# Optimization experiments

Measured on AMD Instinct MI355X. Metric: run time of the kernel, lower is better.

Reference implementation:

```python
import jax, jax.numpy as jnp
import numpy as np

N = 100000
E = 1600000
IN_DIM, H1, H2 = 64, 128, 64


def gcn_conv(x, edge_index, W, b, n_nodes):
    """PyG-style GCNConv: add self-loops, symmetric normalization, x@W, scatter-add, +bias."""
    src, dst = edge_index[0], edge_index[1]
    loop = jnp.arange(n_nodes)
    src = jnp.concatenate([src, loop])
    dst = jnp.concatenate([dst, loop])
    deg = jax.ops.segment_sum(jnp.ones_like(src, dtype=x.dtype), dst, num_segments=n_nodes)
    dinv = jax.lax.rsqrt(deg)  # deg >= 1 due to self loops
    norm = dinv[src] * dinv[dst]  # [E+N]
    xw = x @ W  # [N, out] - transform before gather (out <= in keeps traffic low)
    msg = xw[src] * norm[:, None]  # [E+N, out]
    out = jax.ops.segment_sum(msg, dst, num_segments=n_nodes)
    return out + b


def setup_inputs() -> dict:
    key = jax.random.key(0)
    ks = jax.random.split(key, 8)
    x = jax.random.normal(ks[0], (N, IN_DIM), dtype=jnp.float32)
    edge_index = jax.random.randint(ks[1], (2, E), 0, N, dtype=jnp.int64)
    W1 = jax.random.normal(ks[2], (IN_DIM, H1), dtype=jnp.float32) / np.sqrt(IN_DIM)
    b1 = jnp.zeros((H1,), dtype=jnp.float32)
    W2 = jax.random.normal(ks[3], (H1, H2), dtype=jnp.float32) / np.sqrt(H1)
    b2 = jnp.zeros((H2,), dtype=jnp.float32)
    Wfc = jax.random.normal(ks[4], (H2, 1), dtype=jnp.float32) / np.sqrt(H2)
    bfc = jnp.zeros((1,), dtype=jnp.float32)
    return {"x": x, "edge_index": edge_index, "W1": W1, "b1": b1,
            "W2": W2, "b2": b2, "Wfc": Wfc, "bfc": bfc}


def reference(x, edge_index, W1, b1, W2, b2, Wfc, bfc):
    h = jax.nn.relu(gcn_conv(x, edge_index, W1, b1, N))
    h = jax.nn.relu(gcn_conv(h, edge_index, W2, b2, N))
    return (h @ Wfc + bfc).reshape(-1)  # [N]
```

## Files before the change

kernel.cpp:

```cpp
#include <hip/hip_runtime.h>


constexpr int NN = 100000;
constexpr int NE = 1600000;
constexpr int D0 = 64;
constexpr int D1 = 128;
constexpr int D2 = 64;
constexpr int NB = (NN + 255) / 256;
constexpr int TILE = 8192;
constexpr int H1STRIDE = 132;

typedef unsigned short u16;
typedef unsigned int u32;
typedef __attribute__((ext_vector_type(8))) short short8;
typedef __attribute__((ext_vector_type(4))) float f32x4;
typedef _Float16 h4 __attribute__((ext_vector_type(4)));


__global__ __launch_bounds__(256) void k_zero_b(int* __restrict__ g) {
    int i = blockIdx.x * 256 + threadIdx.x;
    if (i < 512) g[i] = 0;
}

__global__ __launch_bounds__(256) void k_bcount(const int* __restrict__ dst,
                                                int* __restrict__ gbcnt) {
    __shared__ int cnt_s[NB];
    int tid = threadIdx.x;
    int e0 = blockIdx.x * TILE;
    int ecnt = NE - e0 < TILE ? NE - e0 : TILE;
    for (int i = tid; i < NB; i += 256) cnt_s[i] = 0;
    __syncthreads();
    for (int i = tid; i < ecnt; i += 256)
        atomicAdd(&cnt_s[dst[e0 + i] >> 8], 1);
    __syncthreads();
    for (int i = tid; i < NB; i += 256) {
        int c = cnt_s[i];
        if (c) atomicAdd(&gbcnt[i], c);
    }
}

__global__ __launch_bounds__(512) void k_scan_bsum(const int* __restrict__ gbcnt,
                                                   int* __restrict__ bsum,
                                                   int* __restrict__ gcur) {
    __shared__ int s[512];
    int tid = threadIdx.x;
    int v = (tid < NB) ? gbcnt[tid] : 0;
    s[tid] = v;
    __syncthreads();
#pragma unroll
    for (int off = 1; off < 512; off <<= 1) {
        int t = (tid >= off) ? s[tid - off] : 0;
        __syncthreads();
        s[tid] += t;
        __syncthreads();
    }
    int ex = s[tid] - v;
    if (tid <= NB) bsum[tid] = ex;
    if (tid < NB) gcur[tid] = ex;
}

__global__ __launch_bounds__(256) void k_part(const int* __restrict__ src,
                                              const int* __restrict__ dst,
                                              int* __restrict__ gcur,
                                              unsigned* __restrict__ packed) {
    __shared__ int cnt_s[NB];
    __shared__ int gbase_s[NB];
    __shared__ int cur_s[NB];
    int tid = threadIdx.x;
    int e0 = blockIdx.x * TILE;
    int ecnt = NE - e0 < TILE ? NE - e0 : TILE;
    for (int i = tid; i < NB; i += 256) cnt_s[i] = 0;
    __syncthreads();
    for (int i = tid; i < ecnt; i += 256)
        atomicAdd(&cnt_s[dst[e0 + i] >> 8], 1);
    __syncthreads();
    for (int i = tid; i < NB; i += 256) {
        int c = cnt_s[i];
        gbase_s[i] = c ? atomicAdd(&gcur[i], c) : 0;
        cur_s[i] = 0;
    }
    __syncthreads();
    for (int i = tid; i < ecnt; i += 256) {
        int d = dst[e0 + i];
        int s = src[e0 + i];
        int b = d >> 8;
        int slot = atomicAdd(&cur_s[b], 1);
        packed[gbase_s[b] + slot] = ((unsigned)(d & 255) << 24) | (unsigned)s;
    }
}

__global__ __launch_bounds__(256) void k_bucket(const int* __restrict__ bsum,
                                                const unsigned* __restrict__ packed,
                                                int* __restrict__ rowptr,
                                                float* __restrict__ dinv,
                                                int* __restrict__ col) {
    __shared__ int hist[256];
    __shared__ int s[256];
    __shared__ int cur[256];
    int b = blockIdx.x;
    int tid = threadIdx.x;
    int e0 = bsum[b], e1 = bsum[b + 1];
    hist[tid] = 0;
    __syncthreads();
    for (int e = e0 + tid; e < e1; e += 256)
        atomicAdd(&hist[packed[e] >> 24], 1);
    __syncthreads();
    int v = hist[tid];
    int n = (b << 8) + tid;
    if (n < NN) dinv[n] = rsqrtf((float)(v + 1));
    s[tid] = v;
    __syncthreads();
#pragma unroll
    for (int off = 1; off < 256; off <<= 1) {
        int t = (tid >= off) ? s[tid - off] : 0;
        __syncthreads();
        s[tid] += t;
        __syncthreads();
    }
    int base = e0 + s[tid] - v;
    if (n <= NN) rowptr[n] = base;
    cur[tid] = base;
    __syncthreads();
    for (int e = e0 + tid; e < e1; e += 256) {
        unsigned p = packed[e];
        int pos = atomicAdd(&cur[p >> 24], 1);
        col[pos] = (int)((p & 0xFFFFFFu) << 7);
    }
}


__device__ __forceinline__ float4 scale4(const float4& a, float s) {
    return float4{a.x * s, a.y * s, a.z * s, a.w * s};
}

__device__ __forceinline__ void addh8(float4& a, float4& b, uint4 u) {
    h4 h0 = *(h4*)&u.x;
    h4 h1 = *(h4*)&u.z;
    a.x += (float)h0[0]; a.y += (float)h0[1]; a.z += (float)h0[2]; a.w += (float)h0[3];
    b.x += (float)h1[0]; b.y += (float)h1[1]; b.z += (float)h1[2]; b.w += (float)h1[3];
}

__device__ __forceinline__ uint2 packh4(const float4& v) {
    h4 h;
    h[0] = (_Float16)v.x; h[1] = (_Float16)v.y;
    h[2] = (_Float16)v.z; h[3] = (_Float16)v.w;
    return *(uint2*)&h;
}

__device__ __forceinline__ void xor_reduce8(float4& a, float4& b, int mask) {
    a.x += __shfl_xor(a.x, mask, 64);
    a.y += __shfl_xor(a.y, mask, 64);
    a.z += __shfl_xor(a.z, mask, 64);
    a.w += __shfl_xor(a.w, mask, 64);
    b.x += __shfl_xor(b.x, mask, 64);
    b.y += __shfl_xor(b.y, mask, 64);
    b.z += __shfl_xor(b.z, mask, 64);
    b.w += __shfl_xor(b.w, mask, 64);
}

__device__ __forceinline__ u16 f2bf(float f) {
    u32 u = __float_as_uint(f);
    return (u16)((u + 0x7fffu + ((u >> 16) & 1u)) >> 16);
}
__device__ __forceinline__ float bf2f(u16 h) {
    return __uint_as_float(((u32)h) << 16);
}

__global__ __launch_bounds__(256) void k_prescale(const float* __restrict__ x,
                                                  const float* __restrict__ dinv,
                                                  u16* __restrict__ xs) {
    int i = blockIdx.x * 256 + threadIdx.x;
    if (i >= NN * 16) return;
    float di = dinv[i >> 4];
    ((uint2*)xs)[i] = packh4(scale4(((const float4*)x)[i], di));
}

__global__ __launch_bounds__(256) void k_gather1x(const int* __restrict__ rowptr,
                                                  const int* __restrict__ colb,
                                                  const u16* __restrict__ xs,
                                                  const float* __restrict__ dinv,
                                                  float* __restrict__ agg) {
    int wave = (blockIdx.x * 256 + threadIdx.x) >> 6;
    int lane = threadIdx.x & 63;
    if (wave >= NN) return;
    int f8 = lane & 7;
    int es = lane >> 3;
    int r0 = rowptr[wave], r1 = rowptr[wave + 1];
    const char* xsb = (const char*)xs + f8 * 16;
    float4 accA{0, 0, 0, 0}, accB{0, 0, 0, 0};
    if (es == 0) addh8(accA, accB, *(const uint4*)(xsb + (size_t)wave * 128));
    int e = r0 + es;
    for (; e + 8 < r1; e += 16) {
        int c0 = colb[e];
        int c1 = colb[e + 8];
        uint4 v0 = *(const uint4*)(xsb + c0);
        uint4 v1 = *(const uint4*)(xsb + c1);
        addh8(accA, accB, v0);
        addh8(accA, accB, v1);
    }
    for (; e < r1; e += 8)
        addh8(accA, accB, *(const uint4*)(xsb + colb[e]));
    xor_reduce8(accA, accB, 8);
    xor_reduce8(accA, accB, 16);
    xor_reduce8(accA, accB, 32);
    if (es == 0) {
        float di = dinv[wave];
        float4* ag = (float4*)agg + (size_t)wave * 16 + f8 * 2;
        ag[0] = scale4(accA, di);
        ag[1] = scale4(accB, di);
    }
}

__global__ __launch_bounds__(256) void k_splitW(const float* __restrict__ W1,
                                                const float* __restrict__ W2,
                                                u16* __restrict__ W1h, u16* __restrict__ W1l,
                                                u16* __restrict__ W2h, u16* __restrict__ W2l) {
    int i = blockIdx.x * 256 + threadIdx.x;
    if (i >= 8192) return;
    int j = i & 7;
    int l = (i >> 3) & 63;
    int ts = i >> 9;
    int kf = ((l >> 4) << 3) + j;
    int cl = l & 15;
    {
        int s = ts >> 3, t = ts & 7;
        float w = W1[(s * 32 + kf) * D1 + t * 16 + cl];
        u16 h = f2bf(w);
        W1h[i] = h;
        W1l[i] = f2bf(w - bf2f(h));
    }
    {
        int s = ts >> 2, t = ts & 3;
        float w = W2[(s * 32 + kf) * D2 + t * 16 + cl];
        u16 h = f2bf(w);
        W2h[i] = h;
        W2l[i] = f2bf(w - bf2f(h));
    }
}

__global__ __launch_bounds__(256) void k_gemm12(const float* __restrict__ agg,
                                                const u16* __restrict__ W1h,
                                                const u16* __restrict__ W1l,
                                                const float* __restrict__ b1,
                                                const u16* __restrict__ W2h,
                                                const u16* __restrict__ W2l,
                                                const float* __restrict__ dinv,
                                                u16* __restrict__ y2) {
    __shared__ u32 h1s[64 * H1STRIDE];
    int tid = threadIdx.x;
    int l = tid & 63;
    int wv = tid >> 6;
    int n_base = blockIdx.x * 64;
    int row_a = l & 15;
    int kg = (l >> 4) << 3;
    int crow = (l >> 4) * 4;

    short8 Ah[2], Al[2];
#pragma unroll
    for (int s = 0; s < 2; ++s) {
        int an = n_base + wv * 16 + row_a;
        if (an >= NN) an = NN - 1;
        const float* ap = agg + (size_t)an * D0 + s * 32 + kg;
        f32x4 v0 = *(const f32x4*)ap;
        f32x4 v1 = *(const f32x4*)(ap + 4);
#pragma unroll
        for (int j = 0; j < 4; ++j) {
            u16 h0 = f2bf(v0[j]);
            Ah[s][j] = (short)h0;
            Al[s][j] = (short)f2bf(v0[j] - bf2f(h0));
            u16 h1b = f2bf(v1[j]);
            Ah[s][j + 4] = (short)h1b;
            Al[s][j + 4] = (short)f2bf(v1[j] - bf2f(h1b));
        }
    }
#pragma unroll
    for (int t = 0; t < 8; ++t) {
        f32x4 acc = {0.f, 0.f, 0.f, 0.f};
#pragma unroll
        for (int s = 0; s < 2; ++s) {
            short8 Bh = *(const short8*)(W1h + ((size_t)(s * 8 + t) * 64 + l) * 8);
            short8 Bl = *(const short8*)(W1l + ((size_t)(s * 8 + t) * 64 + l) * 8);
            acc = __builtin_amdgcn_mfma_f32_16x16x32_bf16(Ah[s], Bh, acc, 0, 0, 0);
            acc = __builtin_amdgcn_mfma_f32_16x16x32_bf16(Ah[s], Bl, acc, 0, 0, 0);
            acc = __builtin_amdgcn_mfma_f32_16x16x32_bf16(Al[s], Bh, acc, 0, 0, 0);
        }
        float bb = b1[t * 16 + (l & 15)];
        int kcol = t * 16 + (l & 15);
#pragma unroll
        for (int r = 0; r < 4; ++r) {
            int row = wv * 16 + crow + r;
            float v = fmaxf(acc[r] + bb, 0.f);
            u16 h = f2bf(v);
            u16 lo = f2bf(v - bf2f(h));
            h1s[row * H1STRIDE + kcol] = (u32)h | ((u32)lo << 16);
        }
    }
    __syncthreads();

    short8 A2h[4], A2l[4];
#pragma unroll
    for (int s = 0; s < 4; ++s) {
        int row = wv * 16 + row_a;
        const u32* hp = &h1s[row * H1STRIDE + s * 32 + kg];
        uint4 p0 = *(const uint4*)hp;
        uint4 p1 = *(const uint4*)(hp + 4);
        u32 pv[8] = {p0.x, p0.y, p0.z, p0.w, p1.x, p1.y, p1.z, p1.w};
#pragma unroll
        for (int j = 0; j < 8; ++j) {
            A2h[s][j] = (short)(pv[j] & 0xffffu);
            A2l[s][j] = (short)(pv[j] >> 16);
        }
    }
#pragma unroll
    for (int t = 0; t < 4; ++t) {
        f32x4 acc = {0.f, 0.f, 0.f, 0.f};
#pragma unroll
        for (int s = 0; s < 4; ++s) {
            short8 Bh = *(const short8*)(W2h + ((size_t)(s * 4 + t) * 64 + l) * 8);
            short8 Bl = *(const short8*)(W2l + ((size_t)(s * 4 + t) * 64 + l) * 8);
            acc = __builtin_amdgcn_mfma_f32_16x16x32_bf16(A2h[s], Bh, acc, 0, 0, 0);
            acc = __builtin_amdgcn_mfma_f32_16x16x32_bf16(A2h[s], Bl, acc, 0, 0, 0);
            acc = __builtin_amdgcn_mfma_f32_16x16x32_bf16(A2l[s], Bh, acc, 0, 0, 0);
        }
#pragma unroll
        for (int r = 0; r < 4; ++r) {
            int n = n_base + wv * 16 + crow + r;
            if (n < NN) {
                _Float16 hf = (_Float16)(acc[r] * dinv[n]);
                y2[(size_t)n * D2 + t * 16 + (l & 15)] = *(u16*)&hf;
            }
        }
    }
}

__global__ __launch_bounds__(256) void k_gather2_final(const int* __restrict__ rowptr,
                                                       const int* __restrict__ colb,
                                                       const u16* __restrict__ y2,
                                                       const float* __restrict__ dinv,
                                                       const float* __restrict__ b2,
                                                       const float* __restrict__ Wfc,
                                                       const float* __restrict__ bfc,
                                                       float* __restrict__ out) {
    int wave = (blockIdx.x * 256 + threadIdx.x) >> 6;
    int lane = threadIdx.x & 63;
    if (wave >= NN) return;
    int f8 = lane & 7;
    int es = lane >> 3;
    int r0 = rowptr[wave], r1 = rowptr[wave + 1];
    const char* y2b = (const char*)y2 + f8 * 16;
    float4 accA{0, 0, 0, 0}, accB{0, 0, 0, 0};
    if (es == 0) addh8(accA, accB, *(const uint4*)(y2b + (size_t)wave * 128));
    int e = r0 + es;
    for (; e + 8 < r1; e += 16) {
        int c0 = colb[e];
        int c1 = colb[e + 8];
        uint4 v0 = *(const uint4*)(y2b + c0);
        uint4 v1 = *(const uint4*)(y2b + c1);
        addh8(accA, accB, v0);
        addh8(accA, accB, v1);
    }
    for (; e < r1; e += 8)
        addh8(accA, accB, *(const uint4*)(y2b + colb[e]));
    xor_reduce8(accA, accB, 8);
    xor_reduce8(accA, accB, 16);
    xor_reduce8(accA, accB, 32);
    float di = dinv[wave];
    float4 bA = ((const float4*)b2)[f8 * 2];
    float4 bB = ((const float4*)b2)[f8 * 2 + 1];
    float4 wA = ((const float4*)Wfc)[f8 * 2];
    float4 wB = ((const float4*)Wfc)[f8 * 2 + 1];
    float p = fmaxf(fmaf(accA.x, di, bA.x), 0.f) * wA.x
            + fmaxf(fmaf(accA.y, di, bA.y), 0.f) * wA.y
            + fmaxf(fmaf(accA.z, di, bA.z), 0.f) * wA.z
            + fmaxf(fmaf(accA.w, di, bA.w), 0.f) * wA.w
            + fmaxf(fmaf(accB.x, di, bB.x), 0.f) * wB.x
            + fmaxf(fmaf(accB.y, di, bB.y), 0.f) * wB.y
            + fmaxf(fmaf(accB.z, di, bB.z), 0.f) * wB.z
            + fmaxf(fmaf(accB.w, di, bB.w), 0.f) * wB.w;
    p += __shfl_xor(p, 1, 64);
    p += __shfl_xor(p, 2, 64);
    p += __shfl_xor(p, 4, 64);
    if (lane == 0) out[wave] = p + bfc[0];
}

extern "C" void kernel_launch(void* const* d_in, const int* in_sizes, int n_in,
                              void* d_out, int out_size, void* d_ws, size_t ws_size,
                              hipStream_t stream) {
    const float* x   = (const float*)d_in[0];
    const int*   ei  = (const int*)d_in[1];
    const float* W1  = (const float*)d_in[2];
    const float* b1  = (const float*)d_in[3];
    const float* W2  = (const float*)d_in[4];
    const float* b2  = (const float*)d_in[5];
    const float* Wfc = (const float*)d_in[6];
    const float* bfc = (const float*)d_in[7];
    float* out = (float*)d_out;

    const int* src = ei;
    const int* dst = ei + NE;

    char* ws = (char*)d_ws;
    size_t o = 0;
    auto alloc = [&](size_t bytes) { char* p = ws + o; o += (bytes + 255) & ~size_t(255); return p; };
    int*   scratch = (int*)alloc(NN * 4);
    int*   rowptr = (int*)alloc((NN + 1) * 4);
    int*   bsum   = (int*)alloc(512 * 4);
    int*   gcur   = (int*)alloc(NB * 4);
    float* dinv   = (float*)alloc(NN * 4);
    int*   col    = (int*)alloc((size_t)NE * 4);
    u16*   xs     = (u16*)alloc((size_t)NN * D0 * 2);
    float* agg1x  = (float*)alloc((size_t)NN * D0 * 4);
    u16*   y2     = (u16*)alloc((size_t)NN * D2 * 2);
    unsigned* packed = (unsigned*)agg1x;
    int* gbcnt = scratch;
    u16* W1h = (u16*)(scratch + 512);
    u16* W1l = W1h + 8192;
    u16* W2h = W1l + 8192;
    u16* W2l = W2h + 8192;

    const int NT = (NE + TILE - 1) / TILE;

    k_zero_b    <<<2, 256, 0, stream>>>(gbcnt);
    k_splitW    <<<32, 256, 0, stream>>>(W1, W2, W1h, W1l, W2h, W2l);
    k_bcount    <<<NT, 256, 0, stream>>>(dst, gbcnt);
    k_scan_bsum <<<1, 512, 0, stream>>>(gbcnt, bsum, gcur);
    k_part      <<<NT, 256, 0, stream>>>(src, dst, gcur, packed);
    k_bucket    <<<NB, 256, 0, stream>>>(bsum, packed, rowptr, dinv, col);
    k_prescale  <<<(NN * 16 + 255) / 256, 256, 0, stream>>>(x, dinv, xs);

    k_gather1x  <<<(NN * 64 + 255) / 256, 256, 0, stream>>>(rowptr, col, xs, dinv, agg1x);
    k_gemm12    <<<(NN + 63) / 64, 256, 0, stream>>>(agg1x, W1h, W1l, b1, W2h, W2l, dinv, y2);
    k_gather2_final<<<(NN * 64 + 255) / 256, 256, 0, stream>>>(rowptr, col, y2, dinv,
                                                               b2, Wfc, bfc, out);
}
```

Before: 249.7 us.

## Slice feature dimension into 16-wide planes for cache-friendly gathers

```diff
diff --git a/kernel.cpp b/kernel.cpp
--- a/kernel.cpp
+++ b/kernel.cpp
@@ -9,6 +9,7 @@
 constexpr int NB = (NN + 255) / 256;
 constexpr int TILE = 8192;
 constexpr int H1STRIDE = 132;
+constexpr int NH = NN / 2;
 
 typedef unsigned short u16;
 typedef unsigned int u32;
@@ -124,7 +125,7 @@
     for (int e = e0 + tid; e < e1; e += 256) {
         unsigned p = packed[e];
         int pos = atomicAdd(&cur[p >> 24], 1);
-        col[pos] = (int)((p & 0xFFFFFFu) << 7);
+        col[pos] = (int)((p & 0xFFFFFFu) << 5);
     }
 }
 
@@ -171,43 +172,51 @@
                                                   u16* __restrict__ xs) {
     int i = blockIdx.x * 256 + threadIdx.x;
     if (i >= NN * 16) return;
-    float di = dinv[i >> 4];
-    ((uint2*)xs)[i] = packh4(scale4(((const float4*)x)[i], di));
-}
-
-__global__ __launch_bounds__(256) void k_gather1x(const int* __restrict__ rowptr,
+    int n = i >> 4;
+    int k4 = i & 15;
+    int q = k4 >> 2;
+    float di = dinv[n];
+    uint2 v = packh4(scale4(((const float4*)x)[i], di));
+    ((uint2*)xs)[((size_t)q * NN + n) * 4 + (k4 & 3)] = v;
+}
+
+__global__ __launch_bounds__(256) void k_gather1s(const int* __restrict__ rowptr,
                                                   const int* __restrict__ colb,
                                                   const u16* __restrict__ xs,
                                                   const float* __restrict__ dinv,
                                                   float* __restrict__ agg) {
-    int wave = (blockIdx.x * 256 + threadIdx.x) >> 6;
-    int lane = threadIdx.x & 63;
-    if (wave >= NN) return;
-    int f8 = lane & 7;
-    int es = lane >> 3;
-    int r0 = rowptr[wave], r1 = rowptr[wave + 1];
-    const char* xsb = (const char*)xs + f8 * 16;
-    float4 accA{0, 0, 0, 0}, accB{0, 0, 0, 0};
-    if (es == 0) addh8(accA, accB, *(const uint4*)(xsb + (size_t)wave * 128));
+    int bid = blockIdx.x;
+    int sh = bid & 7;
+    int s = sh >> 1, h = sh & 1;
+    int tid = threadIdx.x;
+    int lane = tid & 63;
+    int wv = tid >> 6;
+    int n = h * NH + (bid >> 3) * 32 + wv * 8 + (lane >> 3);
+    if (n >= (h + 1) * NH) return;
+    int half = lane & 1;
+    int es = (lane >> 1) & 3;
+    int r0 = rowptr[n], r1 = rowptr[n + 1];
+    const char* base = (const char*)xs + (size_t)s * NN * 32 + half * 16;
+    float4 a{0, 0, 0, 0}, b{0, 0, 0, 0};
+    if (es == 0) addh8(a, b, *(const uint4*)(base + (size_t)n * 32));
     int e = r0 + es;
-    for (; e + 8 < r1; e += 16) {
+    for (; e + 4 < r1; e += 8) {
         int c0 = colb[e];
-        int c1 = colb[e + 8];
-        uint4 v0 = *(const uint4*)(xsb + c0);
-        uint4 v1 = *(const uint4*)(xsb + c1);
-        addh8(accA, accB, v0);
-        addh8(accA, accB, v1);
-    }
-    for (; e < r1; e += 8)
-        addh8(accA, accB, *(const uint4*)(xsb + colb[e]));
-    xor_reduce8(accA, accB, 8);
-    xor_reduce8(accA, accB, 16);
-    xor_reduce8(accA, accB, 32);
+        int c1 = colb[e + 4];
+        uint4 v0 = *(const uint4*)(base + c0);
+        uint4 v1 = *(const uint4*)(base + c1);
+        addh8(a, b, v0);
+        addh8(a, b, v1);
+    }
+    for (; e < r1; e += 4)
+        addh8(a, b, *(const uint4*)(base + colb[e]));
+    xor_reduce8(a, b, 2);
+    xor_reduce8(a, b, 4);
     if (es == 0) {
-        float di = dinv[wave];
-        float4* ag = (float4*)agg + (size_t)wave * 16 + f8 * 2;
-        ag[0] = scale4(accA, di);
-        ag[1] = scale4(accB, di);
+        float di = dinv[n];
+        float* ag = agg + ((size_t)s * NN + n) * 16 + half * 8;
+        *(float4*)ag = scale4(a, di);
+        *(float4*)(ag + 4) = scale4(b, di);
     }
 }
 
@@ -260,7 +269,9 @@
     for (int s = 0; s < 2; ++s) {
         int an = n_base + wv * 16 + row_a;
         if (an >= NN) an = NN - 1;
-        const float* ap = agg + (size_t)an * D0 + s * 32 + kg;
+        int q = (s * 32 + kg) >> 4;
+        int off = kg & 8;
+        const float* ap = agg + ((size_t)q * NN + an) * 16 + off;
         f32x4 v0 = *(const f32x4*)ap;
         f32x4 v1 = *(const f32x4*)(ap + 4);
 #pragma unroll
@@ -327,60 +338,71 @@
             int n = n_base + wv * 16 + crow + r;
             if (n < NN) {
                 _Float16 hf = (_Float16)(acc[r] * dinv[n]);
-                y2[(size_t)n * D2 + t * 16 + (l & 15)] = *(u16*)&hf;
+                y2[((size_t)t * NN + n) * 16 + (l & 15)] = *(u16*)&hf;
             }
         }
     }
 }
 
-__global__ __launch_bounds__(256) void k_gather2_final(const int* __restrict__ rowptr,
-                                                       const int* __restrict__ colb,
-                                                       const u16* __restrict__ y2,
-                                                       const float* __restrict__ dinv,
-                                                       const float* __restrict__ b2,
-                                                       const float* __restrict__ Wfc,
-                                                       const float* __restrict__ bfc,
-                                                       float* __restrict__ out) {
-    int wave = (blockIdx.x * 256 + threadIdx.x) >> 6;
-    int lane = threadIdx.x & 63;
-    if (wave >= NN) return;
-    int f8 = lane & 7;
-    int es = lane >> 3;
-    int r0 = rowptr[wave], r1 = rowptr[wave + 1];
-    const char* y2b = (const char*)y2 + f8 * 16;
-    float4 accA{0, 0, 0, 0}, accB{0, 0, 0, 0};
-    if (es == 0) addh8(accA, accB, *(const uint4*)(y2b + (size_t)wave * 128));
+__global__ __launch_bounds__(256) void k_gather2s(const int* __restrict__ rowptr,
+                                                  const int* __restrict__ colb,
+                                                  const u16* __restrict__ y2,
+                                                  const float* __restrict__ dinv,
+                                                  const float* __restrict__ b2,
+                                                  const float* __restrict__ Wfc,
+                                                  float* __restrict__ partial) {
+    int bid = blockIdx.x;
+    int sh = bid & 7;
+    int s = sh >> 1, h = sh & 1;
+    int tid = threadIdx.x;
+    int lane = tid & 63;
+    int wv = tid >> 6;
+    int n = h * NH + (bid >> 3) * 32 + wv * 8 + (lane >> 3);
+    if (n >= (h + 1) * NH) return;
+    int half = lane & 1;
+    int es = (lane >> 1) & 3;
+    int r0 = rowptr[n], r1 = rowptr[n + 1];
+    const char* base = (const char*)y2 + (size_t)s * NN * 32 + half * 16;
+    float4 a{0, 0, 0, 0}, b{0, 0, 0, 0};
+    if (es == 0) addh8(a, b, *(const uint4*)(base + (size_t)n * 32));
     int e = r0 + es;
-    for (; e + 8 < r1; e += 16) {
+    for (; e + 4 < r1; e += 8) {
         int c0 = colb[e];
-        int c1 = colb[e + 8];
-        uint4 v0 = *(const uint4*)(y2b + c0);
-        uint4 v1 = *(const uint4*)(y2b + c1);
-        addh8(accA, accB, v0);
-        addh8(accA, accB, v1);
-    }
-    for (; e < r1; e += 8)
-        addh8(accA, accB, *(const uint4*)(y2b + colb[e]));
-    xor_reduce8(accA, accB, 8);
-    xor_reduce8(accA, accB, 16);
-    xor_reduce8(accA, accB, 32);
-    float di = dinv[wave];
-    float4 bA = ((const float4*)b2)[f8 * 2];
-    float4 bB = ((const float4*)b2)[f8 * 2 + 1];
-    float4 wA = ((const float4*)Wfc)[f8 * 2];
-    float4 wB = ((const float4*)Wfc)[f8 * 2 + 1];
-    float p = fmaxf(fmaf(accA.x, di, bA.x), 0.f) * wA.x
-            + fmaxf(fmaf(accA.y, di, bA.y), 0.f) * wA.y
-            + fmaxf(fmaf(accA.z, di, bA.z), 0.f) * wA.z
-            + fmaxf(fmaf(accA.w, di, bA.w), 0.f) * wA.w
-            + fmaxf(fmaf(accB.x, di, bB.x), 0.f) * wB.x
-            + fmaxf(fmaf(accB.y, di, bB.y), 0.f) * wB.y
-            + fmaxf(fmaf(accB.z, di, bB.z), 0.f) * wB.z
-            + fmaxf(fmaf(accB.w, di, bB.w), 0.f) * wB.w;
+        int c1 = colb[e + 4];
+        uint4 v0 = *(const uint4*)(base + c0);
+        uint4 v1 = *(const uint4*)(base + c1);
+        addh8(a, b, v0);
+        addh8(a, b, v1);
+    }
+    for (; e < r1; e += 4)
+        addh8(a, b, *(const uint4*)(base + colb[e]));
+    xor_reduce8(a, b, 2);
+    xor_reduce8(a, b, 4);
+    float di = dinv[n];
+    int fo = s * 16 + half * 8;
+    float4 b0 = *(const float4*)(b2 + fo);
+    float4 b1v = *(const float4*)(b2 + fo + 4);
+    float4 w0 = *(const float4*)(Wfc + fo);
+    float4 w1 = *(const float4*)(Wfc + fo + 4);
+    float p = fmaxf(fmaf(a.x, di, b0.x), 0.f) * w0.x
+            + fmaxf(fmaf(a.y, di, b0.y), 0.f) * w0.y
+            + fmaxf(fmaf(a.z, di, b0.z), 0.f) * w0.z
+            + fmaxf(fmaf(a.w, di, b0.w), 0.f) * w0.w
+            + fmaxf(fmaf(b.x, di, b1v.x), 0.f) * w1.x
+            + fmaxf(fmaf(b.y, di, b1v.y), 0.f) * w1.y
+            + fmaxf(fmaf(b.z, di, b1v.z), 0.f) * w1.z
+            + fmaxf(fmaf(b.w, di, b1v.w), 0.f) * w1.w;
     p += __shfl_xor(p, 1, 64);
-    p += __shfl_xor(p, 2, 64);
-    p += __shfl_xor(p, 4, 64);
-    if (lane == 0) out[wave] = p + bfc[0];
+    if ((lane & 7) == 0 && es == 0) partial[(size_t)s * NN + n] = p;
+}
+
+__global__ __launch_bounds__(256) void k_head(const float* __restrict__ partial,
+                                              const float* __restrict__ bfc,
+                                              float* __restrict__ out) {
+    int i = blockIdx.x * 256 + threadIdx.x;
+    if (i >= NN) return;
+    out[i] = partial[i] + partial[NN + i] + partial[2 * NN + i]
+           + partial[3 * NN + i] + bfc[0];
 }
 
 extern "C" void kernel_launch(void* const* d_in, const int* in_sizes, int n_in,
@@ -411,6 +433,7 @@
     u16*   xs     = (u16*)alloc((size_t)NN * D0 * 2);
     float* agg1x  = (float*)alloc((size_t)NN * D0 * 4);
     u16*   y2     = (u16*)alloc((size_t)NN * D2 * 2);
+    float* partial= (float*)alloc((size_t)NN * 4 * 4);
     unsigned* packed = (unsigned*)agg1x;
     int* gbcnt = scratch;
     u16* W1h = (u16*)(scratch + 512);
@@ -419,6 +442,7 @@
     u16* W2l = W2h + 8192;
 
     const int NT = (NE + TILE - 1) / TILE;
+    const int GB = 8 * ((NH + 31) / 32);
 
     k_zero_b    <<<2, 256, 0, stream>>>(gbcnt);
     k_splitW    <<<32, 256, 0, stream>>>(W1, W2, W1h, W1l, W2h, W2l);
@@ -428,8 +452,8 @@
     k_bucket    <<<NB, 256, 0, stream>>>(bsum, packed, rowptr, dinv, col);
     k_prescale  <<<(NN * 16 + 255) / 256, 256, 0, stream>>>(x, dinv, xs);
 
-    k_gather1x  <<<(NN * 64 + 255) / 256, 256, 0, stream>>>(rowptr, col, xs, dinv, agg1x);
+    k_gather1s  <<<GB, 256, 0, stream>>>(rowptr, col, xs, dinv, agg1x);
     k_gemm12    <<<(NN + 63) / 64, 256, 0, stream>>>(agg1x, W1h, W1l, b1, W2h, W2l, dinv, y2);
-    k_gather2_final<<<(NN * 64 + 255) / 256, 256, 0, stream>>>(rowptr, col, y2, dinv,
-                                                               b2, Wfc, bfc, out);
-}
+    k_gather2s  <<<GB, 256, 0, stream>>>(rowptr, col, y2, dinv, b2, Wfc, partial);
+    k_head      <<<(NN + 255) / 256, 256, 0, stream>>>(partial, bfc, out);
+}
```

Result: no change. 248.0 us (median of 2 runs) (-0.7%).

## Quantize gathered node features to int8 with per-row scales

Applied to the files above, without the earlier changes.

```diff
diff --git a/kernel.cpp b/kernel.cpp
--- a/kernel.cpp
+++ b/kernel.cpp
@@ -14,7 +14,6 @@
 typedef unsigned int u32;
 typedef __attribute__((ext_vector_type(8))) short short8;
 typedef __attribute__((ext_vector_type(4))) float f32x4;
-typedef _Float16 h4 __attribute__((ext_vector_type(4)));
 
 
 __global__ __launch_bounds__(256) void k_zero_b(int* __restrict__ g) {
@@ -124,39 +123,10 @@
     for (int e = e0 + tid; e < e1; e += 256) {
         unsigned p = packed[e];
         int pos = atomicAdd(&cur[p >> 24], 1);
-        col[pos] = (int)((p & 0xFFFFFFu) << 7);
-    }
-}
-
-
-__device__ __forceinline__ float4 scale4(const float4& a, float s) {
-    return float4{a.x * s, a.y * s, a.z * s, a.w * s};
-}
-
-__device__ __forceinline__ void addh8(float4& a, float4& b, uint4 u) {
-    h4 h0 = *(h4*)&u.x;
-    h4 h1 = *(h4*)&u.z;
-    a.x += (float)h0[0]; a.y += (float)h0[1]; a.z += (float)h0[2]; a.w += (float)h0[3];
-    b.x += (float)h1[0]; b.y += (float)h1[1]; b.z += (float)h1[2]; b.w += (float)h1[3];
-}
-
-__device__ __forceinline__ uint2 packh4(const float4& v) {
-    h4 h;
-    h[0] = (_Float16)v.x; h[1] = (_Float16)v.y;
-    h[2] = (_Float16)v.z; h[3] = (_Float16)v.w;
-    return *(uint2*)&h;
-}
-
-__device__ __forceinline__ void xor_reduce8(float4& a, float4& b, int mask) {
-    a.x += __shfl_xor(a.x, mask, 64);
-    a.y += __shfl_xor(a.y, mask, 64);
-    a.z += __shfl_xor(a.z, mask, 64);
-    a.w += __shfl_xor(a.w, mask, 64);
-    b.x += __shfl_xor(b.x, mask, 64);
-    b.y += __shfl_xor(b.y, mask, 64);
-    b.z += __shfl_xor(b.z, mask, 64);
-    b.w += __shfl_xor(b.w, mask, 64);
-}
+        col[pos] = (int)((p & 0xFFFFFFu) << 6);
+    }
+}
+
 
 __device__ __forceinline__ u16 f2bf(float f) {
     u32 u = __float_as_uint(f);
@@ -166,48 +136,86 @@
     return __uint_as_float(((u32)h) << 16);
 }
 
-__global__ __launch_bounds__(256) void k_prescale(const float* __restrict__ x,
+__device__ __forceinline__ void addq8(float* acc, uint2 d, float s) {
+#pragma unroll
+    for (int j = 0; j < 4; ++j) {
+        int v0 = ((int)(d.x << (24 - 8 * j))) >> 24;
+        int v1 = ((int)(d.y << (24 - 8 * j))) >> 24;
+        acc[j]     = fmaf(s, (float)v0, acc[j]);
+        acc[4 + j] = fmaf(s, (float)v1, acc[4 + j]);
+    }
+}
+
+__global__ __launch_bounds__(256) void k_prequant(const float* __restrict__ x,
                                                   const float* __restrict__ dinv,
-                                                  u16* __restrict__ xs) {
-    int i = blockIdx.x * 256 + threadIdx.x;
-    if (i >= NN * 16) return;
-    float di = dinv[i >> 4];
-    ((uint2*)xs)[i] = packh4(scale4(((const float4*)x)[i], di));
-}
-
-__global__ __launch_bounds__(256) void k_gather1x(const int* __restrict__ rowptr,
+                                                  u32* __restrict__ xq,
+                                                  float* __restrict__ xscl) {
+    int n = (blockIdx.x * 256 + threadIdx.x) >> 6;
+    int lane = threadIdx.x & 63;
+    if (n >= NN) return;
+    float v = x[(size_t)n * D0 + lane] * dinv[n];
+    float a = fabsf(v);
+#pragma unroll
+    for (int m = 1; m < 64; m <<= 1) a = fmaxf(a, __shfl_xor(a, m, 64));
+    float scale = a * (1.f / 127.f);
+    float inv = (a > 0.f) ? 127.f / a : 0.f;
+    int q = (int)rintf(v * inv);
+    int cl = lane & 15;
+    u32 w = ((u32)__shfl(q, cl * 4 + 0, 64) & 255u)
+          | (((u32)__shfl(q, cl * 4 + 1, 64) & 255u) << 8)
+          | (((u32)__shfl(q, cl * 4 + 2, 64) & 255u) << 16)
+          | (((u32)__shfl(q, cl * 4 + 3, 64) & 255u) << 24);
+    if (lane < 16) xq[(size_t)n * 16 + cl] = w;
+    if (lane == 0) xscl[n] = scale;
+}
+
+__global__ __launch_bounds__(256) void k_gather1q(const int* __restrict__ rowptr,
                                                   const int* __restrict__ colb,
-                                                  const u16* __restrict__ xs,
+                                                  const u32* __restrict__ xq,
+                                                  const float* __restrict__ xscl,
                                                   const float* __restrict__ dinv,
                                                   float* __restrict__ agg) {
     int wave = (blockIdx.x * 256 + threadIdx.x) >> 6;
     int lane = threadIdx.x & 63;
     if (wave >= NN) return;
-    int f8 = lane & 7;
+    int f = lane & 7;
     int es = lane >> 3;
     int r0 = rowptr[wave], r1 = rowptr[wave + 1];
-    const char* xsb = (const char*)xs + f8 * 16;
-    float4 accA{0, 0, 0, 0}, accB{0, 0, 0, 0};
-    if (es == 0) addh8(accA, accB, *(const uint4*)(xsb + (size_t)wave * 128));
+    const char* base = (const char*)xq + f * 8;
+    float acc[8] = {0, 0, 0, 0, 0, 0, 0, 0};
+    if (es == 0) {
+        int cb = wave << 6;
+        addq8(acc, *(const uint2*)(base + cb), xscl[wave]);
+    }
     int e = r0 + es;
     for (; e + 8 < r1; e += 16) {
         int c0 = colb[e];
         int c1 = colb[e + 8];
-        uint4 v0 = *(const uint4*)(xsb + c0);
-        uint4 v1 = *(const uint4*)(xsb + c1);
-        addh8(accA, accB, v0);
-        addh8(accA, accB, v1);
-    }
-    for (; e < r1; e += 8)
-        addh8(accA, accB, *(const uint4*)(xsb + colb[e]));
-    xor_reduce8(accA, accB, 8);
-    xor_reduce8(accA, accB, 16);
-    xor_reduce8(accA, accB, 32);
+        uint2 d0 = *(const uint2*)(base + c0);
+        uint2 d1 = *(const uint2*)(base + c1);
+        float s0 = xscl[c0 >> 6];
+        float s1 = xscl[c1 >> 6];
+        addq8(acc, d0, s0);
+        addq8(acc, d1, s1);
+    }
+    for (; e < r1; e += 8) {
+        int c = colb[e];
+        uint2 d = *(const uint2*)(base + c);
+        addq8(acc, d, xscl[c >> 6]);
+    }
+#pragma unroll
+    for (int j = 0; j < 8; ++j) {
+        acc[j] += __shfl_xor(acc[j], 8, 64);
+        acc[j] += __shfl_xor(acc[j], 16, 64);
+        acc[j] += __shfl_xor(acc[j], 32, 64);
+    }
     if (es == 0) {
         float di = dinv[wave];
-        float4* ag = (float4*)agg + (size_t)wave * 16 + f8 * 2;
-        ag[0] = scale4(accA, di);
-        ag[1] = scale4(accB, di);
+        float* ag = agg + (size_t)wave * D0 + f * 8;
+        f32x4 v0 = {acc[0] * di, acc[1] * di, acc[2] * di, acc[3] * di};
+        f32x4 v1 = {acc[4] * di, acc[5] * di, acc[6] * di, acc[7] * di};
+        *(f32x4*)ag = v0;
+        *(f32x4*)(ag + 4) = v1;
     }
 }
 
@@ -245,7 +253,8 @@
                                                 const u16* __restrict__ W2h,
                                                 const u16* __restrict__ W2l,
                                                 const float* __restrict__ dinv,
-                                                u16* __restrict__ y2) {
+                                                char* __restrict__ y2q,
+                                                float* __restrict__ y2scl) {
     __shared__ u32 h1s[64 * H1STRIDE];
     int tid = threadIdx.x;
     int l = tid & 63;
@@ -254,6 +263,7 @@
     int row_a = l & 15;
     int kg = (l >> 4) << 3;
     int crow = (l >> 4) * 4;
+    int cl = l & 15;
 
     short8 Ah[2], Al[2];
 #pragma unroll
@@ -284,8 +294,8 @@
             acc = __builtin_amdgcn_mfma_f32_16x16x32_bf16(Ah[s], Bl, acc, 0, 0, 0);
             acc = __builtin_amdgcn_mfma_f32_16x16x32_bf16(Al[s], Bh, acc, 0, 0, 0);
         }
-        float bb = b1[t * 16 + (l & 15)];
-        int kcol = t * 16 + (l & 15);
+        float bb = b1[t * 16 + cl];
+        int kcol = t * 16 + cl;
 #pragma unroll
         for (int r = 0; r < 4; ++r) {
             int row = wv * 16 + crow + r;
@@ -311,6 +321,7 @@
             A2l[s][j] = (short)(pv[j] >> 16);
         }
     }
+    f32x4 accs[4];
 #pragma unroll
     for (int t = 0; t < 4; ++t) {
         f32x4 acc = {0.f, 0.f, 0.f, 0.f};
@@ -322,61 +333,88 @@
             acc = __builtin_amdgcn_mfma_f32_16x16x32_bf16(A2h[s], Bl, acc, 0, 0, 0);
             acc = __builtin_amdgcn_mfma_f32_16x16x32_bf16(A2l[s], Bh, acc, 0, 0, 0);
         }
-#pragma unroll
-        for (int r = 0; r < 4; ++r) {
-            int n = n_base + wv * 16 + crow + r;
-            if (n < NN) {
-                _Float16 hf = (_Float16)(acc[r] * dinv[n]);
-                y2[(size_t)n * D2 + t * 16 + (l & 15)] = *(u16*)&hf;
-            }
-        }
-    }
-}
-
-__global__ __launch_bounds__(256) void k_gather2_final(const int* __restrict__ rowptr,
-                                                       const int* __restrict__ colb,
-                                                       const u16* __restrict__ y2,
-                                                       const float* __restrict__ dinv,
-                                                       const float* __restrict__ b2,
-                                                       const float* __restrict__ Wfc,
-                                                       const float* __restrict__ bfc,
-                                                       float* __restrict__ out) {
+        accs[t] = acc;
+    }
+#pragma unroll
+    for (int r = 0; r < 4; ++r) {
+        int n = n_base + wv * 16 + crow + r;
+        bool ok = n < NN;
+        float di = dinv[ok ? n : 0];
+        float v0 = accs[0][r] * di, v1 = accs[1][r] * di;
+        float v2 = accs[2][r] * di, v3 = accs[3][r] * di;
+        float m = fmaxf(fmaxf(fabsf(v0), fabsf(v1)), fmaxf(fabsf(v2), fabsf(v3)));
+        m = fmaxf(m, __shfl_xor(m, 1, 64));
+        m = fmaxf(m, __shfl_xor(m, 2, 64));
+        m = fmaxf(m, __shfl_xor(m, 4, 64));
+        m = fmaxf(m, __shfl_xor(m, 8, 64));
+        float inv = (m > 0.f) ? 127.f / m : 0.f;
+        if (ok) {
+            if (cl == 0) y2scl[n] = m * (1.f / 127.f);
+            char* yr = y2q + (size_t)n * D2 + cl;
+            yr[0]  = (char)(int)rintf(v0 * inv);
+            yr[16] = (char)(int)rintf(v1 * inv);
+            yr[32] = (char)(int)rintf(v2 * inv);
+            yr[48] = (char)(int)rintf(v3 * inv);
+        }
+    }
+}
+
+__global__ __launch_bounds__(256) void k_gather2q(const int* __restrict__ rowptr,
+                                                  const int* __restrict__ colb,
+                                                  const u32* __restrict__ y2q,
+                                                  const float* __restrict__ y2scl,
+                                                  const float* __restrict__ dinv,
+                                                  const float* __restrict__ b2,
+                                                  const float* __restrict__ Wfc,
+                                                  const float* __restrict__ bfc,
+                                                  float* __restrict__ out) {
     int wave = (blockIdx.x * 256 + threadIdx.x) >> 6;
     int lane = threadIdx.x & 63;
     if (wave >= NN) return;
-    int f8 = lane & 7;
+    int f = lane & 7;
     int es = lane >> 3;
     int r0 = rowptr[wave], r1 = rowptr[wave + 1];
-    const char* y2b = (const char*)y2 + f8 * 16;
-    float4 accA{0, 0, 0, 0}, accB{0, 0, 0, 0};
-    if (es == 0) addh8(accA, accB, *(const uint4*)(y2b + (size_t)wave * 128));
+    const char* base = (const char*)y2q + f * 8;
+    float acc[8] = {0, 0, 0, 0, 0, 0, 0, 0};
+    if (es == 0) {
+        int cb = wave << 6;
+        addq8(acc, *(const uint2*)(base + cb), y2scl[wave]);
+    }
     int e = r0 + es;
     for (; e + 8 < r1; e += 16) {
         int c0 = colb[e];
         int c1 = colb[e + 8];
-        uint4 v0 = *(const uint4*)(y2b + c0);
-        uint4 v1 = *(const uint4*)(y2b + c1);
-        addh8(accA, accB, v0);
-        addh8(accA, accB, v1);
-    }
-    for (; e < r1; e += 8)
-        addh8(accA, accB, *(const uint4*)(y2b + colb[e]));
-    xor_reduce8(accA, accB, 8);
-    xor_reduce8(accA, accB, 16);
-    xor_reduce8(accA, accB, 32);
+        uint2 d0 = *(const uint2*)(base + c0);
+        uint2 d1 = *(const uint2*)(base + c1);
+        float s0 = y2scl[c0 >> 6];
+        float s1 = y2scl[c1 >> 6];
+        addq8(acc, d0, s0);
+        addq8(acc, d1, s1);
+    }
+    for (; e < r1; e += 8) {
+        int c = colb[e];
+        uint2 d = *(const uint2*)(base + c);
+        addq8(acc, d, y2scl[c >> 6]);
+    }
+#pragma unroll
+    for (int j = 0; j < 8; ++j) {
+        acc[j] += __shfl_xor(acc[j], 8, 64);
+        acc[j] += __shfl_xor(acc[j], 16, 64);
+        acc[j] += __shfl_xor(acc[j], 32, 64);
+    }
     float di = dinv[wave];
-    float4 bA = ((const float4*)b2)[f8 * 2];
-    float4 bB = ((const float4*)b2)[f8 * 2 + 1];
-    float4 wA = ((const float4*)Wfc)[f8 * 2];
-    float4 wB = ((const float4*)Wfc)[f8 * 2 + 1];
-    float p = fmaxf(fmaf(accA.x, di, bA.x), 0.f) * wA.x
-            + fmaxf(fmaf(accA.y, di, bA.y), 0.f) * wA.y
-            + fmaxf(fmaf(accA.z, di, bA.z), 0.f) * wA.z
-            + fmaxf(fmaf(accA.w, di, bA.w), 0.f) * wA.w
-            + fmaxf(fmaf(accB.x, di, bB.x), 0.f) * wB.x
-            + fmaxf(fmaf(accB.y, di, bB.y), 0.f) * wB.y
-            + fmaxf(fmaf(accB.z, di, bB.z), 0.f) * wB.z
-            + fmaxf(fmaf(accB.w, di, bB.w), 0.f) * wB.w;
+    f32x4 b0 = *(const f32x4*)(b2 + f * 8);
+    f32x4 b1v = *(const f32x4*)(b2 + f * 8 + 4);
+    f32x4 w0 = *(const f32x4*)(Wfc + f * 8);
+    f32x4 w1 = *(const f32x4*)(Wfc + f * 8 + 4);
+    float p = fmaxf(fmaf(acc[0], di, b0[0]), 0.f) * w0[0]
+            + fmaxf(fmaf(acc[1], di, b0[1]), 0.f) * w0[1]
+            + fmaxf(fmaf(acc[2], di, b0[2]), 0.f) * w0[2]
+            + fmaxf(fmaf(acc[3], di, b0[3]), 0.f) * w0[3]
+            + fmaxf(fmaf(acc[4], di, b1v[0]), 0.f) * w1[0]
+            + fmaxf(fmaf(acc[5], di, b1v[1]), 0.f) * w1[1]
+            + fmaxf(fmaf(acc[6], di, b1v[2]), 0.f) * w1[2]
+            + fmaxf(fmaf(acc[7], di, b1v[3]), 0.f) * w1[3];
     p += __shfl_xor(p, 1, 64);
     p += __shfl_xor(p, 2, 64);
     p += __shfl_xor(p, 4, 64);
@@ -408,9 +446,11 @@
     int*   gcur   = (int*)alloc(NB * 4);
     float* dinv   = (float*)alloc(NN * 4);
     int*   col    = (int*)alloc((size_t)NE * 4);
-    u16*   xs     = (u16*)alloc((size_t)NN * D0 * 2);
+    u32*   xq     = (u32*)alloc((size_t)NN * D0);
+    float* xscl   = (float*)alloc(NN * 4);
     float* agg1x  = (float*)alloc((size_t)NN * D0 * 4);
-    u16*   y2     = (u16*)alloc((size_t)NN * D2 * 2);
+    char*  y2q    = (char*)alloc((size_t)NN * D2);
+    float* y2scl  = (float*)alloc(NN * 4);
     unsigned* packed = (unsigned*)agg1x;
     int* gbcnt = scratch;
     u16* W1h = (u16*)(scratch + 512);
@@ -426,10 +466,11 @@
     k_scan_bsum <<<1, 512, 0, stream>>>(gbcnt, bsum, gcur);
     k_part      <<<NT, 256, 0, stream>>>(src, dst, gcur, packed);
     k_bucket    <<<NB, 256, 0, stream>>>(bsum, packed, rowptr, dinv, col);
-    k_prescale  <<<(NN * 16 + 255) / 256, 256, 0, stream>>>(x, dinv, xs);
-
-    k_gather1x  <<<(NN * 64 + 255) / 256, 256, 0, stream>>>(rowptr, col, xs, dinv, agg1x);
-    k_gemm12    <<<(NN + 63) / 64, 256, 0, stream>>>(agg1x, W1h, W1l, b1, W2h, W2l, dinv, y2);
-    k_gather2_final<<<(NN * 64 + 255) / 256, 256, 0, stream>>>(rowptr, col, y2, dinv,
-                                                               b2, Wfc, bfc, out);
-}
+    k_prequant  <<<(NN * 64 + 255) / 256, 256, 0, stream>>>(x, dinv, xq, xscl);
+
+    k_gather1q  <<<(NN * 64 + 255) / 256, 256, 0, stream>>>(rowptr, col, xq, xscl, dinv, agg1x);
+    k_gemm12    <<<(NN + 63) / 64, 256, 0, stream>>>(agg1x, W1h, W1l, b1, W2h, W2l, dinv,
+                                                     y2q, y2scl);
+    k_gather2q  <<<(NN * 64 + 255) / 256, 256, 0, stream>>>(rowptr, col, (const u32*)y2q,
+                                                            y2scl, dinv, b2, Wfc, bfc, out);
+}
```

New measurement: 261.6 us. +4.8%, slower.
